# Kernel optimization log

Hardware: AMD Instinct MI355X
Metric: run time of the kernel (lower is better)

## Reference

```python
import jax, jax.numpy as jnp
import numpy as np

B, S, K = 32, 256, 6
D, H, DK, DV = 768, 12, 64, 64
DFF, L, A, V, MAXLEN = 3072, 12, 128, 30000, 256
EPS = 1e-5


def setup_inputs() -> dict:
    key = jax.random.key(0)
    ks = jax.random.split(key, 32)
    n = lambda k, shp: (jax.random.normal(k, shp, dtype=jnp.float32) * 0.02)
    inp = {
        "input_ids": jax.random.randint(ks[0], (B, S, K), 0, V, dtype=jnp.int32),
        "input_ids_origin": jax.random.randint(ks[1], (B, S), 0, V, dtype=jnp.int32),
        "tok_embed": n(ks[2], (V, D)),
        "pos_embed": n(ks[3], (MAXLEN, D)),
        "sa_W": n(ks[4], (D, A)), "sa_b": jnp.zeros((A,), jnp.float32),
        "sm_W": n(ks[5], (A, 1)), "sm_b": jnp.zeros((1,), jnp.float32),
        "Wq": n(ks[6], (L, D, H * DK)), "bq": jnp.zeros((L, H * DK), jnp.float32),
        "Wk": n(ks[7], (L, D, H * DK)), "bk": jnp.zeros((L, H * DK), jnp.float32),
        "Wv": n(ks[8], (L, D, H * DV)), "bv": jnp.zeros((L, H * DV), jnp.float32),
        "Wo": n(ks[9], (L, H * DV, D)), "bo": jnp.zeros((L, D), jnp.float32),
        "ln_g": jnp.ones((L, D), jnp.float32), "ln_b": jnp.zeros((L, D), jnp.float32),
        "f1W": n(ks[10], (L, D, DFF)), "f1b": jnp.zeros((L, DFF), jnp.float32),
        "f2W": n(ks[11], (L, DFF, D)), "f2b": jnp.zeros((L, D), jnp.float32),
        "t1W": n(ks[12], (D, D // 2)), "t1b": jnp.zeros((D // 2,), jnp.float32),
        "t2W": n(ks[13], (D // 2, 2)), "t2b": jnp.zeros((2,), jnp.float32),
    }
    return inp


def _layernorm(x, g, b):
    mu = jnp.mean(x, axis=-1, keepdims=True)
    var = jnp.mean(jnp.square(x - mu), axis=-1, keepdims=True)
    return (x - mu) * jax.lax.rsqrt(var + EPS) * g + b


def reference(input_ids, input_ids_origin, tok_embed, pos_embed, sa_W, sa_b, sm_W, sm_b,
              Wq, bq, Wk, bk, Wv, bv, Wo, bo, ln_g, ln_b, f1W, f1b, f2W, f2b,
              t1W, t1b, t2W, t2b):
    # batched k-mer embedding + soft-attention pooling (vectorizes the per-position loop)
    emb = tok_embed[input_ids]                                   # [B,S,K,D]
    h = (emb @ sa_W + sa_b) @ sm_W + sm_b                        # [B,S,K,1]
    alphas = jax.nn.softmax(h, axis=2)                           # exp/sum over kmer dim
    x = jnp.sum(emb * alphas, axis=2)                            # [B,S,D]
    x = x + pos_embed[:S][None, :, :]
    # pad mask on keys: [B,1,1,S] broadcast to [B,H,S,S]
    mask = (input_ids_origin == 0)[:, None, None, :]
    scale = 1.0 / np.sqrt(DK)
    for l in range(L):
        q = (x @ Wq[l] + bq[l]).reshape(B, S, H, DK)
        k = (x @ Wk[l] + bk[l]).reshape(B, S, H, DK)
        v = (x @ Wv[l] + bv[l]).reshape(B, S, H, DV)
        scores = jnp.einsum('bqhd,bkhd->bhqk', q, k) * scale
        scores = jnp.where(mask, -1e9, scores)
        attn = jax.nn.softmax(scores, axis=-1)
        ctx = jnp.einsum('bhqk,bkhd->bqhd', attn, v).reshape(B, S, H * DV)
        x = _layernorm(ctx @ Wo[l] + bo[l] + x, ln_g[l], ln_b[l])
        # feed-forward (no residual in the original)
        x = jax.nn.relu(x @ f1W[l] + f1b[l]) @ f2W[l] + f2b[l]
    rep = x[:, 0, :]                                             # [B,D]
    logits = jax.nn.relu(rep @ t1W + t1b) @ t2W + t2b            # [B,2]
    return logits, rep
```

## Files before the change

### kernel.cpp

```cpp
#include <hip/hip_runtime.h>
#include <stdint.h>


typedef unsigned short u16;
typedef __attribute__((ext_vector_type(8))) __bf16 bf16x8;
typedef __attribute__((ext_vector_type(4))) float f4;

__device__ __forceinline__ u16 f2b(float f) {
  union { float f; uint32_t u; } v; v.f = f;
  uint32_t r = v.u + 0x7fffu + ((v.u >> 16) & 1u);
  return (u16)(r >> 16);
}

__device__ __forceinline__ void gload_lds16(const void* g, void* l) {
  __builtin_amdgcn_global_load_lds((const __attribute__((address_space(1))) uint32_t*)g,
                                   (__attribute__((address_space(3))) uint32_t*)l, 16, 0, 0);
}

__device__ __forceinline__ f4 mfma16(bf16x8 a, bf16x8 b, f4 c) {
  return __builtin_amdgcn_mfma_f32_16x16x32_bf16(a, b, c, 0, 0, 0);
}

template<int RELU, int RES, int WF32, int WB16>
__global__ __launch_bounds__(256, 2) void gemm_bt(
    const u16* __restrict__ A, const u16* __restrict__ Bt,
    const float* __restrict__ bias,
    const float* res, float* Cf, u16* Cb,
    int M, int N, int K)
{
  __shared__ __align__(16) u16 As[128 * 32];
  __shared__ __align__(16) u16 Bs[128 * 32];
  const int tid  = threadIdx.x;
  const int lane = tid & 63;
  const int w    = tid >> 6;
  const int wr   = w >> 1, wc = w & 1;
  const int m0   = blockIdx.x * 128;
  const int n0   = blockIdx.y * 128;

  f4 acc[4][4];
  const f4 zf = {0.f, 0.f, 0.f, 0.f};
#pragma unroll
  for (int i = 0; i < 4; ++i)
#pragma unroll
    for (int j = 0; j < 4; ++j) acc[i][j] = zf;

  const int cA  = w * 64 + lane;
  const int rA  = cA >> 2;
  const int kc8 = (cA & 3) * 8;
  const u16* gA0 = A  + (long)(m0 + rA) * K + kc8;
  const u16* gA1 = gA0 + (long)64 * K;
  const u16* gB0 = Bt + (long)(n0 + rA) * K + kc8;
  const u16* gB1 = gB0 + (long)64 * K;
  u16* lA0 = &As[w * 512];
  u16* lA1 = &As[w * 512 + 2048];
  u16* lB0 = &Bs[w * 512];
  u16* lB1 = &Bs[w * 512 + 2048];

  const int rdA = (wr * 64 + (lane & 15)) * 32 + (lane >> 4) * 8;
  const int rdB = (wc * 64 + (lane & 15)) * 32 + (lane >> 4) * 8;

  const int nk = K >> 5;
  for (int kk = 0; kk < nk; ++kk) {
    gload_lds16(gA0, lA0);
    gload_lds16(gA1, lA1);
    gload_lds16(gB0, lB0);
    gload_lds16(gB1, lB1);
    gA0 += 32; gA1 += 32; gB0 += 32; gB1 += 32;
    asm volatile("s_waitcnt vmcnt(0)" ::: "memory");
    __syncthreads();
    bf16x8 af[4], bf[4];
#pragma unroll
    for (int mf = 0; mf < 4; ++mf) af[mf] = *(const bf16x8*)&As[rdA + mf * 512];
#pragma unroll
    for (int nf = 0; nf < 4; ++nf) bf[nf] = *(const bf16x8*)&Bs[rdB + nf * 512];
#pragma unroll
    for (int mf = 0; mf < 4; ++mf)
#pragma unroll
      for (int nf = 0; nf < 4; ++nf)
        acc[mf][nf] = mfma16(af[mf], bf[nf], acc[mf][nf]);
    __syncthreads();
  }

  const int col0 = n0 + wc * 64 + (lane & 15);
  const int row0 = m0 + wr * 64 + (lane >> 4) * 4;
#pragma unroll
  for (int mf = 0; mf < 4; ++mf) {
#pragma unroll
    for (int nf = 0; nf < 4; ++nf) {
      const int col = col0 + nf * 16;
      const float bv = bias[col];
#pragma unroll
      for (int i = 0; i < 4; ++i) {
        const long r = row0 + mf * 16 + i;
        float v = acc[mf][nf][i] + bv;
        if (RES)  v += res[r * N + col];
        if (RELU) v  = fmaxf(v, 0.0f);
        if (WF32) Cf[r * N + col] = v;
        if (WB16) Cb[r * N + col] = f2b(v);
      }
    }
  }
}

__device__ __forceinline__ void trans_tile(const float* __restrict__ src, u16* __restrict__ dst,
                                           int R, int C, int r0, int c0, int tid,
                                           float (*tile)[33])
{
  const int tx = tid & 31, ty = tid >> 5;
#pragma unroll
  for (int i = 0; i < 4; ++i)
    tile[ty + 8 * i][tx] = src[(long)(r0 + ty + 8 * i) * C + (c0 + tx)];
  __syncthreads();
#pragma unroll
  for (int i = 0; i < 4; ++i)
    dst[(long)(c0 + ty + 8 * i) * R + (r0 + tx)] = f2b(tile[tx][ty + 8 * i]);
}

__global__ __launch_bounds__(256) void prep_weights(
    const float* Wq, const float* Wk, const float* Wv, const float* Wo,
    const float* F1, const float* F2,
    u16* WqkvT, u16* WoT, u16* F1T, u16* F2T)
{
  __shared__ float tile[32][33];
  const int bid = blockIdx.x, tid = threadIdx.x;
  if (bid < 1728) {
    const int which = bid / 576, t = bid % 576;
    const float* src = (which == 0) ? Wq : (which == 1) ? Wk : Wv;
    trans_tile(src, WqkvT + (long)which * 768 * 768, 768, 768,
               (t / 24) * 32, (t % 24) * 32, tid, tile);
  } else if (bid < 2304) {
    const int t = bid - 1728;
    trans_tile(Wo, WoT, 768, 768, (t / 24) * 32, (t % 24) * 32, tid, tile);
  } else if (bid < 4608) {
    const int t = bid - 2304;
    trans_tile(F1, F1T, 768, 3072, (t / 96) * 32, (t % 96) * 32, tid, tile);
  } else {
    const int t = bid - 4608;
    trans_tile(F2, F2T, 3072, 768, (t / 24) * 32, (t % 24) * 32, tid, tile);
  }
}

__global__ __launch_bounds__(256) void vtrans(const u16* __restrict__ qkv, u16* __restrict__ vT)
{
  const int bid = blockIdx.x;
  const int bh = bid >> 4, t = bid & 15;
  const int b = bh / 12, h = bh % 12;
  const int tk = (t >> 1) * 32, td = (t & 1) * 32;
  __shared__ u16 tile[32][34];
  const int tx = threadIdx.x & 31, ty = threadIdx.x >> 5;
#pragma unroll
  for (int i = 0; i < 4; ++i)
    tile[ty + 8 * i][tx] = qkv[(long)(b * 256 + tk + ty + 8 * i) * 2304 + 1536 + h * 64 + td + tx];
  __syncthreads();
#pragma unroll
  for (int i = 0; i < 4; ++i)
    vT[((long)(bh * 64 + td + ty + 8 * i)) * 256 + tk + tx] = tile[tx][ty + 8 * i];
}

__global__ __launch_bounds__(256, 2) void attn_kernel(
    const u16* __restrict__ qkv, const u16* __restrict__ vT,
    const int* __restrict__ origin, u16* __restrict__ ctx)
{
  const int bh = blockIdx.x;
  const int b = bh / 12, h = bh % 12;
  const int tid = threadIdx.x, lane = tid & 63, w = tid >> 6;
  const int g = lane >> 4, c = lane & 15;
  __shared__ float mbias[256];
  __shared__ __align__(16) u16 Ps[4][64 * 40];
  mbias[tid] = (origin[b * 256 + tid] == 0) ? -1e9f : 0.0f;
  __syncthreads();

  bf16x8 qf[4][2];
  const long qbase = (long)(b * 256 + w * 64 + c) * 2304 + h * 64;
#pragma unroll
  for (int mf = 0; mf < 4; ++mf)
#pragma unroll
    for (int ks = 0; ks < 2; ++ks)
      qf[mf][ks] = *(const bf16x8*)&qkv[qbase + (long)mf * 16 * 2304 + ks * 32 + g * 8];

  f4 o[4][4];
  float mrun[4][4], lrun[4][4];
  const f4 zf = {0.f, 0.f, 0.f, 0.f};
#pragma unroll
  for (int i = 0; i < 4; ++i)
#pragma unroll
    for (int j = 0; j < 4; ++j) { o[i][j] = zf; mrun[i][j] = -1e30f; lrun[i][j] = 0.f; }

  u16* ps = Ps[w];
  const float scale = 0.125f;
  for (int kc = 0; kc < 8; ++kc) {
    bf16x8 kf[2][2];
#pragma unroll
    for (int nf = 0; nf < 2; ++nf)
#pragma unroll
      for (int ks = 0; ks < 2; ++ks)
        kf[nf][ks] = *(const bf16x8*)&qkv[(long)(b * 256 + kc * 32 + nf * 16 + c) * 2304
                                          + 768 + h * 64 + ks * 32 + g * 8];
    f4 s[4][2];
#pragma unroll
    for (int mf = 0; mf < 4; ++mf)
#pragma unroll
      for (int nf = 0; nf < 2; ++nf) {
        f4 t = mfma16(qf[mf][0], kf[nf][0], zf);
        s[mf][nf] = mfma16(qf[mf][1], kf[nf][1], t);
      }
#pragma unroll
    for (int mf = 0; mf < 4; ++mf)
#pragma unroll
      for (int i = 0; i < 4; ++i) {
        float v0 = s[mf][0][i] * scale + mbias[kc * 32 + c];
        float v1 = s[mf][1][i] * scale + mbias[kc * 32 + 16 + c];
        float rm = fmaxf(v0, v1);
        rm = fmaxf(rm, __shfl_xor(rm, 1));
        rm = fmaxf(rm, __shfl_xor(rm, 2));
        rm = fmaxf(rm, __shfl_xor(rm, 4));
        rm = fmaxf(rm, __shfl_xor(rm, 8));
        const float mn   = fmaxf(mrun[mf][i], rm);
        const float corr = __expf(mrun[mf][i] - mn);
        mrun[mf][i] = mn;
        const float p0 = __expf(v0 - mn), p1 = __expf(v1 - mn);
        s[mf][0][i] = p0; s[mf][1][i] = p1;
        float rs = p0 + p1;
        rs += __shfl_xor(rs, 1);
        rs += __shfl_xor(rs, 2);
        rs += __shfl_xor(rs, 4);
        rs += __shfl_xor(rs, 8);
        lrun[mf][i] = lrun[mf][i] * corr + rs;
#pragma unroll
        for (int df = 0; df < 4; ++df) o[mf][df][i] *= corr;
      }
#pragma unroll
    for (int mf = 0; mf < 4; ++mf)
#pragma unroll
      for (int nf = 0; nf < 2; ++nf)
#pragma unroll
        for (int i = 0; i < 4; ++i)
          ps[(mf * 16 + g * 4 + i) * 40 + nf * 16 + c] = f2b(s[mf][nf][i]);
    bf16x8 pa[4], vb[4];
#pragma unroll
    for (int mf = 0; mf < 4; ++mf) pa[mf] = *(const bf16x8*)&ps[(mf * 16 + c) * 40 + g * 8];
#pragma unroll
    for (int df = 0; df < 4; ++df)
      vb[df] = *(const bf16x8*)&vT[(long)(bh * 64 + df * 16 + c) * 256 + kc * 32 + g * 8];
#pragma unroll
    for (int mf = 0; mf < 4; ++mf)
#pragma unroll
      for (int df = 0; df < 4; ++df)
        o[mf][df] = mfma16(pa[mf], vb[df], o[mf][df]);
  }

#pragma unroll
  for (int mf = 0; mf < 4; ++mf)
#pragma unroll
    for (int i = 0; i < 4; ++i) {
      const float inv = 1.0f / lrun[mf][i];
      const long r = (long)(b * 256 + w * 64 + mf * 16 + g * 4 + i);
#pragma unroll
      for (int df = 0; df < 4; ++df)
        ctx[r * 768 + h * 64 + df * 16 + c] = f2b(o[mf][df][i] * inv);
    }
}

__global__ __launch_bounds__(256) void ln_kernel(const float* __restrict__ x,
    const float* __restrict__ gam, const float* __restrict__ bet, u16* __restrict__ out)
{
  const int row = blockIdx.x, tid = threadIdx.x;
  const int lane = tid & 63, w = tid >> 6;
  const float* xr = x + (long)row * 768;
  const float v0 = xr[tid], v1 = xr[tid + 256], v2 = xr[tid + 512];
  float s = v0 + v1 + v2;
#pragma unroll
  for (int off = 1; off < 64; off <<= 1) s += __shfl_xor(s, off);
  __shared__ float r1[4], r2[4];
  if (lane == 0) r1[w] = s;
  __syncthreads();
  const float mu = (r1[0] + r1[1] + r1[2] + r1[3]) * (1.0f / 768.0f);
  const float d0 = v0 - mu, d1 = v1 - mu, d2 = v2 - mu;
  float q = d0 * d0 + d1 * d1 + d2 * d2;
#pragma unroll
  for (int off = 1; off < 64; off <<= 1) q += __shfl_xor(q, off);
  if (lane == 0) r2[w] = q;
  __syncthreads();
  const float var = (r2[0] + r2[1] + r2[2] + r2[3]) * (1.0f / 768.0f);
  const float rs = rsqrtf(var + 1e-5f);
  out[(long)row * 768 + tid]       = f2b(d0 * rs * gam[tid]       + bet[tid]);
  out[(long)row * 768 + tid + 256] = f2b(d1 * rs * gam[tid + 256] + bet[tid + 256]);
  out[(long)row * 768 + tid + 512] = f2b(d2 * rs * gam[tid + 512] + bet[tid + 512]);
}

__global__ void weff_kernel(const float* __restrict__ saW, const float* __restrict__ sab,
                            const float* __restrict__ smW, const float* __restrict__ smb,
                            float* weff, float* beff)
{
  const int d = blockIdx.x * 256 + threadIdx.x;
  float acc = 0.f;
  for (int a = 0; a < 128; ++a) acc += saW[d * 128 + a] * smW[a];
  weff[d] = acc;
  if (d == 0) {
    float bb = smb[0];
    for (int a = 0; a < 128; ++a) bb += sab[a] * smW[a];
    beff[0] = bb;
  }
}

__global__ __launch_bounds__(256) void embed_kernel(
    const int* __restrict__ ids, const float* __restrict__ tok, const float* __restrict__ pos,
    const float* __restrict__ weff, const float* __restrict__ beff,
    float* __restrict__ x, u16* __restrict__ xb)
{
  const int m = blockIdx.x;
  const int s = m & 255;
  const int tid = threadIdx.x, lane = tid & 63, w = tid >> 6;
  __shared__ float emb[6][768];
  __shared__ float hred[6][4];
  const int* idp = ids + m * 6;
  float part[6];
#pragma unroll
  for (int k = 0; k < 6; ++k) {
    const float* e = tok + (long)idp[k] * 768;
    float p = 0.f;
#pragma unroll
    for (int j = 0; j < 3; ++j) {
      const int d = tid + j * 256;
      const float val = e[d];
      emb[k][d] = val;
      p += val * weff[d];
    }
    part[k] = p;
  }
#pragma unroll
  for (int k = 0; k < 6; ++k) {
    float p = part[k];
#pragma unroll
    for (int off = 1; off < 64; off <<= 1) p += __shfl_xor(p, off);
    if (lane == 0) hred[k][w] = p;
  }
  __syncthreads();
  float hv[6], mx = -1e30f;
#pragma unroll
  for (int k = 0; k < 6; ++k) {
    hv[k] = hred[k][0] + hred[k][1] + hred[k][2] + hred[k][3] + beff[0];
    mx = fmaxf(mx, hv[k]);
  }
  float esum = 0.f;
#pragma unroll
  for (int k = 0; k < 6; ++k) { hv[k] = __expf(hv[k] - mx); esum += hv[k]; }
  const float inv = 1.0f / esum;
#pragma unroll
  for (int j = 0; j < 3; ++j) {
    const int d = tid + j * 256;
    float acc = pos[s * 768 + d];
#pragma unroll
    for (int k = 0; k < 6; ++k) acc += hv[k] * inv * emb[k][d];
    x[(long)m * 768 + d] = acc;
    xb[(long)m * 768 + d] = f2b(acc);
  }
}

__global__ void pack_bqkv(const float* __restrict__ bq, const float* __restrict__ bk,
                          const float* __restrict__ bv, float* __restrict__ bqkv)
{
  const int l = blockIdx.x;
  for (int n = threadIdx.x; n < 2304; n += 256) {
    float v = (n < 768) ? bq[l * 768 + n] : (n < 1536) ? bk[l * 768 + n - 768]
                                                       : bv[l * 768 + n - 1536];
    bqkv[l * 2304 + n] = v;
  }
}

__global__ __launch_bounds__(256) void head_kernel(const float* __restrict__ x,
    const float* __restrict__ t1W, const float* __restrict__ t1b,
    const float* __restrict__ t2W, const float* __restrict__ t2b,
    float* __restrict__ out)
{
  const int b = blockIdx.x, tid = threadIdx.x;
  __shared__ float rep[768];
  __shared__ float hbuf[384];
  const float* xr = x + (long)b * 256 * 768;
  for (int d = tid; d < 768; d += 256) {
    const float v = xr[d];
    rep[d] = v;
    out[64 + b * 768 + d] = v;
  }
  __syncthreads();
  for (int j = tid; j < 384; j += 256) {
    float acc = t1b[j];
    for (int d = 0; d < 768; ++d) acc += rep[d] * t1W[(long)d * 384 + j];
    hbuf[j] = fmaxf(acc, 0.0f);
  }
  __syncthreads();
  if (tid < 2) {
    float acc = t2b[tid];
    for (int a = 0; a < 384; ++a) acc += hbuf[a] * t2W[a * 2 + tid];
    out[b * 2 + tid] = acc;
  }
}

extern "C" void kernel_launch(void* const* d_in, const int* in_sizes, int n_in,
                              void* d_out, int out_size, void* d_ws, size_t ws_size,
                              hipStream_t stream) {
  const int*   ids    = (const int*)d_in[0];
  const int*   origin = (const int*)d_in[1];
  const float* tok    = (const float*)d_in[2];
  const float* pos    = (const float*)d_in[3];
  const float* saW    = (const float*)d_in[4];
  const float* sab    = (const float*)d_in[5];
  const float* smW    = (const float*)d_in[6];
  const float* smb    = (const float*)d_in[7];
  const float* Wq     = (const float*)d_in[8];
  const float* bq     = (const float*)d_in[9];
  const float* Wk     = (const float*)d_in[10];
  const float* bk     = (const float*)d_in[11];
  const float* Wv     = (const float*)d_in[12];
  const float* bv     = (const float*)d_in[13];
  const float* Wo     = (const float*)d_in[14];
  const float* bo     = (const float*)d_in[15];
  const float* lng    = (const float*)d_in[16];
  const float* lnb    = (const float*)d_in[17];
  const float* f1W    = (const float*)d_in[18];
  const float* f1b    = (const float*)d_in[19];
  const float* f2W    = (const float*)d_in[20];
  const float* f2bb   = (const float*)d_in[21];
  const float* t1W    = (const float*)d_in[22];
  const float* t1b    = (const float*)d_in[23];
  const float* t2W    = (const float*)d_in[24];
  const float* t2b    = (const float*)d_in[25];
  float* out = (float*)d_out;

  char* ws = (char*)d_ws;
  size_t off = 0;
  auto alloc = [&](size_t bytes) -> void* {
    void* p = ws + off;
    off += (bytes + 255) & ~(size_t)255;
    return p;
  };
  float* weff  = (float*)alloc(768 * 4);
  float* beff  = (float*)alloc(256);
  float* bqkv  = (float*)alloc(12 * 2304 * 4);
  float* x     = (float*)alloc((size_t)8192 * 768 * 4);
  u16*   xb    = (u16*)alloc((size_t)8192 * 768 * 2);
  u16*   big   = (u16*)alloc((size_t)8192 * 3072 * 2);
  u16*   ctx   = (u16*)alloc((size_t)8192 * 768 * 2);
  u16*   vT    = (u16*)alloc((size_t)384 * 64 * 256 * 2);
  u16*   WqkvT = (u16*)alloc((size_t)2304 * 768 * 2);
  u16*   WoT   = (u16*)alloc((size_t)768 * 768 * 2);
  u16*   F1T   = (u16*)alloc((size_t)3072 * 768 * 2);
  u16*   F2T   = (u16*)alloc((size_t)768 * 3072 * 2);

  pack_bqkv<<<12, 256, 0, stream>>>(bq, bk, bv, bqkv);
  weff_kernel<<<3, 256, 0, stream>>>(saW, sab, smW, smb, weff, beff);
  embed_kernel<<<8192, 256, 0, stream>>>(ids, tok, pos, weff, beff, x, xb);

  for (int l = 0; l < 12; ++l) {
    prep_weights<<<6912, 256, 0, stream>>>(
        Wq + (size_t)l * 768 * 768, Wk + (size_t)l * 768 * 768,
        Wv + (size_t)l * 768 * 768, Wo + (size_t)l * 768 * 768,
        f1W + (size_t)l * 768 * 3072, f2W + (size_t)l * 3072 * 768,
        WqkvT, WoT, F1T, F2T);
    gemm_bt<0, 0, 0, 1><<<dim3(64, 18), 256, 0, stream>>>(
        xb, WqkvT, bqkv + l * 2304, nullptr, nullptr, big, 8192, 2304, 768);
    vtrans<<<6144, 256, 0, stream>>>(big, vT);
    attn_kernel<<<384, 256, 0, stream>>>(big, vT, origin, ctx);
    gemm_bt<0, 1, 1, 0><<<dim3(64, 6), 256, 0, stream>>>(
        ctx, WoT, bo + l * 768, x, x, nullptr, 8192, 768, 768);
    ln_kernel<<<8192, 256, 0, stream>>>(x, lng + l * 768, lnb + l * 768, xb);
    gemm_bt<1, 0, 0, 1><<<dim3(64, 24), 256, 0, stream>>>(
        xb, F1T, f1b + l * 3072, nullptr, nullptr, big, 8192, 3072, 768);
    gemm_bt<0, 0, 1, 1><<<dim3(64, 6), 256, 0, stream>>>(
        big, F2T, f2bb + l * 768, nullptr, x, xb, 8192, 768, 3072);
  }

  head_kernel<<<32, 256, 0, stream>>>(x, t1W, t1b, t2W, t2b, out);
}
```

Baseline: 3.609 ms.

## Double-buffer GEMM LDS tiles and XOR-swizzle k-chunks to avoid bank conflicts

The bf16 GEMM now keeps two LDS buffers, so the global-to-LDS load of the next K-slice is issued before the MFMAs on the current slice, overlapping memory latency with compute. This also removes one barrier per iteration. In addition, the 8-element k-chunk position inside each 32-wide row is XOR-swizzled on the store and read sides to reduce LDS bank conflicts. LDS use doubles to 32KB per block, which could limit occupancy at the requested two blocks per CU.

```diff
diff --git a/kernel.cpp b/kernel.cpp
--- a/kernel.cpp
+++ b/kernel.cpp
@@ -28,8 +28,8 @@
     const float* res, float* Cf, u16* Cb,
     int M, int N, int K)
 {
-  __shared__ __align__(16) u16 As[128 * 32];
-  __shared__ __align__(16) u16 Bs[128 * 32];
+  __shared__ __align__(16) u16 As[2][128 * 32];
+  __shared__ __align__(16) u16 Bs[2][128 * 32];
   const int tid  = threadIdx.x;
   const int lane = tid & 63;
   const int w    = tid >> 6;
@@ -46,40 +46,48 @@
 
   const int cA  = w * 64 + lane;
   const int rA  = cA >> 2;
-  const int kc8 = (cA & 3) * 8;
+  const int kc8 = ((cA & 3) ^ ((cA >> 3) & 3)) * 8;
   const u16* gA0 = A  + (long)(m0 + rA) * K + kc8;
   const u16* gA1 = gA0 + (long)64 * K;
   const u16* gB0 = Bt + (long)(n0 + rA) * K + kc8;
   const u16* gB1 = gB0 + (long)64 * K;
-  u16* lA0 = &As[w * 512];
-  u16* lA1 = &As[w * 512 + 2048];
-  u16* lB0 = &Bs[w * 512];
-  u16* lB1 = &Bs[w * 512 + 2048];
-
-  const int rdA = (wr * 64 + (lane & 15)) * 32 + (lane >> 4) * 8;
-  const int rdB = (wc * 64 + (lane & 15)) * 32 + (lane >> 4) * 8;
+
+  const int rdA = (wr * 64 + (lane & 15)) * 32 + (((lane >> 4) ^ ((lane >> 1) & 3))) * 8;
+  const int rdB = (wc * 64 + (lane & 15)) * 32 + (((lane >> 4) ^ ((lane >> 1) & 3))) * 8;
+
+  auto STAGE = [&](int buf) {
+    gload_lds16(gA0, &As[buf][w * 512]);
+    gload_lds16(gA1, &As[buf][w * 512 + 2048]);
+    gload_lds16(gB0, &Bs[buf][w * 512]);
+    gload_lds16(gB1, &Bs[buf][w * 512 + 2048]);
+    gA0 += 32; gA1 += 32; gB0 += 32; gB1 += 32;
+  };
+  auto COMPUTE = [&](int buf) {
+    bf16x8 af[4], bfr[4];
+#pragma unroll
+    for (int mf = 0; mf < 4; ++mf) af[mf] = *(const bf16x8*)&As[buf][rdA + mf * 512];
+#pragma unroll
+    for (int nf = 0; nf < 4; ++nf) bfr[nf] = *(const bf16x8*)&Bs[buf][rdB + nf * 512];
+#pragma unroll
+    for (int mf = 0; mf < 4; ++mf)
+#pragma unroll
+      for (int nf = 0; nf < 4; ++nf)
+        acc[mf][nf] = mfma16(af[mf], bfr[nf], acc[mf][nf]);
+  };
 
   const int nk = K >> 5;
-  for (int kk = 0; kk < nk; ++kk) {
-    gload_lds16(gA0, lA0);
-    gload_lds16(gA1, lA1);
-    gload_lds16(gB0, lB0);
-    gload_lds16(gB1, lB1);
-    gA0 += 32; gA1 += 32; gB0 += 32; gB1 += 32;
+  STAGE(0);
+  asm volatile("s_waitcnt vmcnt(0)" ::: "memory");
+  __syncthreads();
+  int cur = 0;
+  for (int kk = 0; kk < nk - 1; ++kk) {
+    STAGE(cur ^ 1);
+    COMPUTE(cur);
     asm volatile("s_waitcnt vmcnt(0)" ::: "memory");
     __syncthreads();
-    bf16x8 af[4], bf[4];
-#pragma unroll
-    for (int mf = 0; mf < 4; ++mf) af[mf] = *(const bf16x8*)&As[rdA + mf * 512];
-#pragma unroll
-    for (int nf = 0; nf < 4; ++nf) bf[nf] = *(const bf16x8*)&Bs[rdB + nf * 512];
-#pragma unroll
-    for (int mf = 0; mf < 4; ++mf)
-#pragma unroll
-      for (int nf = 0; nf < 4; ++nf)
-        acc[mf][nf] = mfma16(af[mf], bf[nf], acc[mf][nf]);
-    __syncthreads();
-  }
+    cur ^= 1;
+  }
+  COMPUTE(cur);
 
   const int col0 = n0 + wc * 64 + (lane & 15);
   const int row0 = m0 + wr * 64 + (lane >> 4) * 4;
```

Result: no change. 3.587 ms (-0.6%).
